# Optimization experiments

Measured on AMD Instinct MI355X. Metric: run time of the kernel, lower is better.

The kernel has to match this reference:

```python
import jax, jax.numpy as jnp
import numpy as np

TAU = 0.05


def _normalize(x):
    return x / jnp.linalg.norm(x, axis=-1, keepdims=True)


def setup_inputs() -> dict:
    key = jax.random.key(0)
    ks = jax.random.split(key, 7)
    D, S, Q, N, P = 256, 64, 4096, 16384, 1024
    return {
        "article_emb": jax.random.normal(ks[0], (D,), dtype=jnp.float32),
        "section_embs": jax.random.normal(ks[1], (S, D), dtype=jnp.float32),
        "question_embs": jax.random.normal(ks[2], (Q, D), dtype=jnp.float32),
        "sentence_embs": jax.random.normal(ks[3], (N, D), dtype=jnp.float32),
        "paragraph_idx_for_question": jax.random.randint(ks[4], (Q,), 0, P, dtype=jnp.int32),
        "section_idx_for_question": jax.random.randint(ks[5], (Q,), 0, S, dtype=jnp.int32),
        "sent_paragraph_idx": jax.random.randint(ks[6], (N,), 0, P, dtype=jnp.int32),
        "num_paragraphs": P,
    }


def reference(article_emb, section_embs, question_embs, sentence_embs,
              paragraph_idx_for_question, section_idx_for_question,
              sent_paragraph_idx, num_paragraphs):
    tau = TAU
    dt = question_embs.dtype
    # normalize (article is normalized in the original but unused in the loss; AT_loss == 0)
    _ = _normalize(article_emb)
    sec = _normalize(section_embs)   # [S, D]
    que = _normalize(question_embs)  # [Q, D]
    sen = _normalize(sentence_embs)  # [N, D]
    Q, N = que.shape[0], sen.shape[0]
    S = sec.shape[0]

    # ---------- QS debiased InfoNCE ----------
    sim_qs = jnp.matmul(que, sen.T) / tau              # [Q, N]
    exp_qs = jnp.exp(sim_qs)                           # [Q, N]
    pos = paragraph_idx_for_question[:, None] == sent_paragraph_idx[None, :]  # [Q, N]
    M = pos.sum(axis=1)                                # positives per question
    Nn = N - M                                         # negatives per question
    sum_pos = jnp.where(pos, exp_qs, 0.0).sum(axis=1)
    sum_neg = exp_qs.sum(axis=1) - sum_pos
    eta_plus = 1.0 / max(int(num_paragraphs), 1)
    eta_minus = 1.0 - eta_plus
    min_val = jnp.exp(jnp.asarray(-1.0 / tau, dtype=dt))
    M_f = jnp.maximum(M, 1).astype(dt)
    Nn_f = jnp.maximum(Nn, 1).astype(dt)
    g = jnp.maximum((sum_neg / Nn_f - eta_plus * sum_pos / M_f) / eta_minus, min_val)  # [Q]
    valid = (M > 0) & (Nn > 0)                         # [Q]
    # -log(numer / (numer + N_neg * g)) = -(sim - log(denom))
    denom_qs = exp_qs + (Nn.astype(dt) * g)[:, None]
    log_ratio_qs = sim_qs - jnp.log(denom_qs)
    mask_qs = pos & valid[:, None]
    total_qs = jnp.where(valid, M, 0).sum()
    qs_loss = -jnp.where(mask_qs, log_ratio_qs, 0.0).sum()
    qs_loss = jnp.where(total_qs > 0, qs_loss / total_qs.astype(dt), jnp.asarray(0.0, dt))

    # ---------- SQ InfoNCE ----------
    sim_sq = jnp.matmul(sec, que.T) / tau              # [S, Q]
    exp_sq = jnp.exp(sim_sq)
    posq = section_idx_for_question[None, :] == jnp.arange(S)[:, None]  # [S, Q]
    Mq = posq.sum(axis=1)
    Nnq = Q - Mq
    sum_neg_q = exp_sq.sum(axis=1) - jnp.where(posq, exp_sq, 0.0).sum(axis=1)  # [S]
    log_ratio_sq = sim_sq - jnp.log(exp_sq + sum_neg_q[:, None])
    validq = (Mq > 0) & (Nnq > 0)
    mask_sq = posq & validq[:, None]
    total_sq = jnp.where(validq, Mq, 0).sum()
    sq_loss = -jnp.where(mask_sq, log_ratio_sq, 0.0).sum()
    sq_loss = jnp.where(total_sq > 0, sq_loss / total_sq.astype(dt), jnp.asarray(0.0, dt))

    return qs_loss + sq_loss
```

## Files before the change

kernel.cpp:

```cpp
#include <hip/hip_runtime.h>
#include <hip/hip_bf16.h>
#include <math.h>

#define D 256
#define INV_TAU 20.0f
#define CAP 64
#define PBUF 128

typedef __attribute__((ext_vector_type(4))) float f32x4;
typedef __attribute__((ext_vector_type(8))) short bf16x8_t;

#define GLOAD16(gp, lp) \
    __builtin_amdgcn_global_load_lds((const __attribute__((address_space(1))) void*)(gp), \
                                     (__attribute__((address_space(3))) void*)(lp), 16, 0, 0)

__device__ __forceinline__ unsigned short f2bf(float f) {
    union { float f; unsigned u; } v; v.f = f;
    unsigned r = v.u + 0x7FFFu + ((v.u >> 16) & 1u);
    return (unsigned short)(r >> 16);
}

__global__ void norm_all(const float* __restrict__ que, const float* __restrict__ sen,
                         const float* __restrict__ sec,
                         unsigned short* __restrict__ queb, unsigned short* __restrict__ senb,
                         unsigned short* __restrict__ secb, int Q, int N, int S) {
    int r = blockIdx.x * 4 + (threadIdx.x >> 6);
    int lane = threadIdx.x & 63;
    if (r >= Q + N + S) return;
    const float* src; unsigned short* dst; int row;
    if (r < Q) { src = que; dst = queb; row = r; }
    else if (r < Q + N) { src = sen; dst = senb; row = r - Q; }
    else { src = sec; dst = secb; row = r - Q - N; }
    const float4* p = (const float4*)(src + (size_t)row * D);
    float4 v = p[lane];
    float ss = v.x * v.x + v.y * v.y + v.z * v.z + v.w * v.w;
    #pragma unroll
    for (int m = 1; m < 64; m <<= 1) ss += __shfl_xor(ss, m);
    float rn = rsqrtf(ss);
    ushort4 o;
    o.x = f2bf(v.x * rn); o.y = f2bf(v.y * rn); o.z = f2bf(v.z * rn); o.w = f2bf(v.w * rn);
    *(ushort4*)(dst + (size_t)row * D + lane * 4) = o;
}

__global__ __launch_bounds__(256, 4)
void qs_sq(const unsigned short* __restrict__ queb, const unsigned short* __restrict__ senb,
           const unsigned short* __restrict__ secb,
           const int* __restrict__ pidq, const int* __restrict__ pidn,
           const int* __restrict__ sidx, int Q,
           float* __restrict__ partial, int* __restrict__ cnt, float* __restrict__ pos_s,
           float* __restrict__ sq_all, float* __restrict__ sq_pos, int* __restrict__ sq_m,
           float* __restrict__ simq) {
    __shared__ unsigned short As[2][128 * 32];
    __shared__ unsigned short Bs[2][128 * 32];
    __shared__ int pqs[128];
    __shared__ int pns[128];
    __shared__ float sums[2][128];
    __shared__ int lcnt;
    __shared__ int lq[PBUF];
    __shared__ float lsv[PBUF];

    const int tid = threadIdx.x;
    const int lane = tid & 63;
    const int cl = lane & 15;
    const int g = lane >> 4;
    const int wid = tid >> 6;

    if (blockIdx.y == 0) {
        if ((int)blockIdx.x >= (Q >> 7)) return;
        const int q0 = blockIdx.x * 128;
        const int qw = q0 + wid * 32;
        f32x4 acc[4][2];
        #pragma unroll
        for (int si = 0; si < 4; ++si)
            #pragma unroll
            for (int qi = 0; qi < 2; ++qi)
                acc[si][qi] = (f32x4){0.f, 0.f, 0.f, 0.f};
        const unsigned short* abase = secb + (size_t)cl * D + g * 8;
        const unsigned short* bbase = queb + (size_t)(qw + cl) * D + g * 8;
        #pragma unroll
        for (int kk = 0; kk < 8; ++kk) {
            const int k0 = kk * 32;
            bf16x8_t af[4], bq[2];
            #pragma unroll
            for (int si = 0; si < 4; ++si)
                af[si] = *(const bf16x8_t*)(abase + si * 16 * D + k0);
            #pragma unroll
            for (int qi = 0; qi < 2; ++qi)
                bq[qi] = *(const bf16x8_t*)(bbase + qi * 16 * D + k0);
            #pragma unroll
            for (int si = 0; si < 4; ++si)
                #pragma unroll
                for (int qi = 0; qi < 2; ++qi)
                    acc[si][qi] = __builtin_amdgcn_mfma_f32_16x16x32_bf16(af[si], bq[qi], acc[si][qi], 0, 0, 0);
        }
        int sidxv[2];
        sidxv[0] = sidx[qw + cl];
        sidxv[1] = sidx[qw + 16 + cl];
        #pragma unroll
        for (int si = 0; si < 4; ++si) {
            float pa[4] = {0.f, 0.f, 0.f, 0.f};
            #pragma unroll
            for (int qi = 0; qi < 2; ++qi) {
                #pragma unroll
                for (int j = 0; j < 4; ++j) {
                    int srow = si * 16 + g * 4 + j;
                    float sv = acc[si][qi][j] * INV_TAU;
                    float e = __expf(sv);
                    pa[j] += e;
                    if (sidxv[qi] == srow) {
                        int q = qw + qi * 16 + cl;
                        simq[q] = sv;
                        atomicAdd(&sq_pos[srow], e);
                        atomicAdd(&sq_m[srow], 1);
                    }
                }
            }
            #pragma unroll
            for (int j = 0; j < 4; ++j) {
                float a = pa[j];
                #pragma unroll
                for (int msk = 1; msk < 16; msk <<= 1) a += __shfl_xor(a, msk);
                if (cl == 0) atomicAdd(&sq_all[si * 16 + g * 4 + j], a);
            }
        }
        return;
    }

    const int wr = wid >> 1, wc = wid & 1;
    const int n0 = blockIdx.x * 128;
    const int q0 = (blockIdx.y - 1) * 128;

    if (tid < 128) pqs[tid] = pidq[q0 + tid];
    else           pns[tid - 128] = pidn[n0 + tid - 128];
    if (tid == 0) lcnt = 0;
    __syncthreads();

    int cid0 = (2 * wid) * 64 + lane;
    int cid1 = (2 * wid + 1) * 64 + lane;
    const unsigned short* qa0 = queb + (size_t)(q0 + (cid0 >> 2)) * D + (cid0 & 3) * 8;
    const unsigned short* qa1 = queb + (size_t)(q0 + (cid1 >> 2)) * D + (cid1 & 3) * 8;
    const unsigned short* sb0 = senb + (size_t)(n0 + (cid0 >> 2)) * D + (cid0 & 3) * 8;
    const unsigned short* sb1 = senb + (size_t)(n0 + (cid1 >> 2)) * D + (cid1 & 3) * 8;
    const int ld0 = (2 * wid) * 512;
    const int ld1 = (2 * wid + 1) * 512;

#define STAGE(buf, k0) do { \
    GLOAD16(qa0 + (k0), &As[buf][ld0]); \
    GLOAD16(qa1 + (k0), &As[buf][ld1]); \
    GLOAD16(sb0 + (k0), &Bs[buf][ld0]); \
    GLOAD16(sb1 + (k0), &Bs[buf][ld1]); \
} while (0)

    f32x4 acc[4][4];
    #pragma unroll
    for (int m = 0; m < 4; ++m)
        #pragma unroll
        for (int n = 0; n < 4; ++n)
            acc[m][n] = (f32x4){0.f, 0.f, 0.f, 0.f};

    STAGE(0, 0);
    #pragma unroll
    for (int ks = 0; ks < 8; ++ks) {
        const int cur = ks & 1;
        if (ks < 7) {
            STAGE(cur ^ 1, (ks + 1) * 32);
            asm volatile("s_waitcnt vmcnt(4)" ::: "memory");
        } else {
            asm volatile("s_waitcnt vmcnt(0)" ::: "memory");
        }
        __builtin_amdgcn_s_barrier();
        bf16x8_t af[4], bg[4];
        #pragma unroll
        for (int m = 0; m < 4; ++m) {
            int r = wr * 64 + m * 16 + cl;
            af[m] = *(const bf16x8_t*)&As[cur][r * 32 + g * 8];
        }
        #pragma unroll
        for (int n = 0; n < 4; ++n) {
            int r = wc * 64 + n * 16 + cl;
            bg[n] = *(const bf16x8_t*)&Bs[cur][r * 32 + g * 8];
        }
        #pragma unroll
        for (int m = 0; m < 4; ++m)
            #pragma unroll
            for (int n = 0; n < 4; ++n)
                acc[m][n] = __builtin_amdgcn_mfma_f32_16x16x32_bf16(af[m], bg[n], acc[m][n], 0, 0, 0);
        if (ks < 7) __builtin_amdgcn_s_barrier();
    }
#undef STAGE

    #pragma unroll
    for (int m = 0; m < 4; ++m) {
        float se[4] = {0.f, 0.f, 0.f, 0.f};
        int pqr[4];
        #pragma unroll
        for (int j = 0; j < 4; ++j) pqr[j] = pqs[wr * 64 + m * 16 + g * 4 + j];
        #pragma unroll
        for (int n = 0; n < 4; ++n) {
            const int pcol = pns[wc * 64 + n * 16 + cl];
            #pragma unroll
            for (int j = 0; j < 4; ++j) {
                float s = acc[m][n][j] * INV_TAU;
                float e = __expf(s);
                se[j] += e;
                if (pqr[j] == pcol) {
                    int li = atomicAdd(&lcnt, 1);
                    if (li < PBUF) { lq[li] = q0 + wr * 64 + m * 16 + g * 4 + j; lsv[li] = s; }
                }
            }
        }
        #pragma unroll
        for (int j = 0; j < 4; ++j) {
            float a = se[j];
            #pragma unroll
            for (int msk = 1; msk < 16; msk <<= 1) a += __shfl_xor(a, msk);
            if (cl == 0) sums[wc][wr * 64 + m * 16 + g * 4 + j] = a;
        }
    }
    __syncthreads();
    if (tid < 128)
        partial[(size_t)blockIdx.x * Q + q0 + tid] = sums[0][tid] + sums[1][tid];
    int nc = lcnt < PBUF ? lcnt : PBUF;
    for (int i = tid; i < nc; i += 256) {
        int q = lq[i];
        int idx = atomicAdd(&cnt[q], 1);
        if (idx < CAP) pos_s[(size_t)q * CAP + idx] = lsv[i];
    }
}

__global__ __launch_bounds__(256)
void finish(const float* __restrict__ partial, int NB,
            const int* __restrict__ cnt, const float* __restrict__ pos_s,
            const int* __restrict__ sidx, const float* __restrict__ simq,
            const float* __restrict__ sq_all, const float* __restrict__ sq_pos,
            const int* __restrict__ sq_m,
            const int* __restrict__ npp, int Qn, int Ntot,
            float* __restrict__ bpart) {
    __shared__ float fred[4][4];
    const int tid = threadIdx.x, lane = tid & 63, wid = tid >> 6;
    const int q = blockIdx.x * 4 + wid;

    float Sa = 0.f;
    for (int nb = lane; nb < NB; nb += 64) Sa += partial[(size_t)nb * Qn + q];
    #pragma unroll
    for (int m = 1; m < 64; m <<= 1) Sa += __shfl_xor(Sa, m);

    int M = cnt[q];
    int mc = M < CAP ? M : CAP;
    float s = 0.f, e = 0.f;
    if (lane < mc) { s = pos_s[(size_t)q * CAP + lane]; e = __expf(s); }
    float Sp = e;
    #pragma unroll
    for (int m = 1; m < 64; m <<= 1) Sp += __shfl_xor(Sp, m);

    int Nn = Ntot - M;
    int P = npp[0];
    float eta_p = 1.0f / (float)(P > 1 ? P : 1);
    float eta_m = 1.0f - eta_p;
    float Mf = (float)(M > 1 ? M : 1);
    float Nnf = (float)(Nn > 1 ? Nn : 1);
    float gg = fmaxf(((Sa - Sp) / Nnf - eta_p * Sp / Mf) / eta_m, __expf(-INV_TAU));
    float c = (float)Nn * gg;

    float contrib = (lane < mc) ? (s - __logf(e + c)) : 0.f;
    #pragma unroll
    for (int m = 1; m < 64; m <<= 1) contrib += __shfl_xor(contrib, m);

    if (lane == 0) {
        float qs_num = 0.f, qs_cnt = 0.f, sq_num = 0.f, sq_cnt = 0.f;
        if (M > 0 && Nn > 0) { qs_num = contrib; qs_cnt = (float)M; }
        int sct = sidx[q];
        int Mq = sq_m[sct];
        if (Mq > 0 && (Qn - Mq) > 0) {
            float sv = simq[q];
            float sumneg = sq_all[sct] - sq_pos[sct];
            sq_num = sv - __logf(__expf(sv) + sumneg);
            sq_cnt = 1.f;
        }
        fred[wid][0] = qs_num; fred[wid][1] = qs_cnt;
        fred[wid][2] = sq_num; fred[wid][3] = sq_cnt;
    }
    __syncthreads();
    if (tid < 4) {
        float v = fred[0][tid] + fred[1][tid] + fred[2][tid] + fred[3][tid];
        bpart[(size_t)blockIdx.x * 4 + tid] = v;
    }
}

__global__ void combine2(const float* __restrict__ bpart, int nblk, float* __restrict__ out) {
    __shared__ float r2[4][4];
    const int tid = threadIdx.x, lane = tid & 63, wid = tid >> 6;
    float v[4] = {0.f, 0.f, 0.f, 0.f};
    for (int i = tid; i < nblk; i += 256) {
        #pragma unroll
        for (int c2 = 0; c2 < 4; ++c2) v[c2] += bpart[(size_t)i * 4 + c2];
    }
    #pragma unroll
    for (int m = 1; m < 64; m <<= 1)
        #pragma unroll
        for (int c2 = 0; c2 < 4; ++c2) v[c2] += __shfl_xor(v[c2], m);
    if (lane == 0) {
        #pragma unroll
        for (int c2 = 0; c2 < 4; ++c2) r2[wid][c2] = v[c2];
    }
    __syncthreads();
    if (tid == 0) {
        float qs_num = r2[0][0] + r2[1][0] + r2[2][0] + r2[3][0];
        float qs_cnt = r2[0][1] + r2[1][1] + r2[2][1] + r2[3][1];
        float sq_num = r2[0][2] + r2[1][2] + r2[2][2] + r2[3][2];
        float sq_cnt = r2[0][3] + r2[1][3] + r2[2][3] + r2[3][3];
        float qs = qs_cnt > 0.f ? -qs_num / qs_cnt : 0.f;
        float sq = sq_cnt > 0.f ? -sq_num / sq_cnt : 0.f;
        out[0] = qs + sq;
    }
}

extern "C" void kernel_launch(void* const* d_in, const int* in_sizes, int n_in,
                              void* d_out, int out_size, void* d_ws, size_t ws_size,
                              hipStream_t stream) {
    const float* sec = (const float*)d_in[1];
    const float* que = (const float*)d_in[2];
    const float* sen = (const float*)d_in[3];
    const int* pidq = (const int*)d_in[4];
    const int* sidx = (const int*)d_in[5];
    const int* pidn = (const int*)d_in[6];
    const int* npp = (const int*)d_in[7];
    const int S = in_sizes[1] / D;
    const int Q = in_sizes[2] / D;
    const int N = in_sizes[3] / D;
    const int NB = N / 128;
    const int FBLK = Q / 4;

    char* p = (char*)d_ws;
    unsigned short* queb = (unsigned short*)p; p += (size_t)Q * D * 2;
    unsigned short* senb = (unsigned short*)p; p += (size_t)N * D * 2;
    unsigned short* secb = (unsigned short*)p; p += (size_t)S * D * 2;
    float* simq = (float*)p; p += (size_t)Q * 4;
    float* pos_s = (float*)p; p += (size_t)Q * CAP * 4;
    float* partial = (float*)p; p += (size_t)NB * Q * 4;
    float* bpart = (float*)p; p += (size_t)FBLK * 4 * 4;
    char* z0 = p;
    int* cnt = (int*)p; p += (size_t)Q * 4;
    float* sq_all = (float*)p; p += (size_t)S * 4;
    float* sq_pos = (float*)p; p += (size_t)S * 4;
    int* sq_m = (int*)p; p += (size_t)S * 4;
    size_t zbytes = (size_t)(p - z0);

    hipMemsetAsync(z0, 0, zbytes, stream);
    norm_all<<<(Q + N + S + 3) / 4, 256, 0, stream>>>(que, sen, sec, queb, senb, secb, Q, N, S);
    qs_sq<<<dim3(NB, Q / 128 + 1), 256, 0, stream>>>(queb, senb, secb, pidq, pidn, sidx, Q,
                                                     partial, cnt, pos_s,
                                                     sq_all, sq_pos, sq_m, simq);
    finish<<<FBLK, 256, 0, stream>>>(partial, NB, cnt, pos_s, sidx, simq,
                                     sq_all, sq_pos, sq_m, npp, Q, N, bpart);
    combine2<<<1, 256, 0, stream>>>(bpart, FBLK, (float*)d_out);
}
```

Before: 100.6 us.

## Widen QS GEMM tile to 128x256 and XOR-swizzle LDS layout

Doubles the sentence dimension of each QS block tile from 128 to 256 columns, so every wave computes a 64x128 sub-tile with 32 MFMA accumulators and the question tile is reused across twice as many sentences. Global-to-LDS loads and LDS fragment reads now use an XOR swizzle on the 16-byte chunk index to cut LDS bank conflicts. Launch bounds drop to 2 waves per SIMD to fit the larger register footprint. The grid and per-block partial count halve, which reduces parallelism and occupancy in exchange for more reuse.

```diff
diff --git a/kernel.cpp b/kernel.cpp
--- a/kernel.cpp
+++ b/kernel.cpp
@@ -42,7 +42,7 @@
     *(ushort4*)(dst + (size_t)row * D + lane * 4) = o;
 }
 
-__global__ __launch_bounds__(256, 4)
+__global__ __launch_bounds__(256, 2)
 void qs_sq(const unsigned short* __restrict__ queb, const unsigned short* __restrict__ senb,
            const unsigned short* __restrict__ secb,
            const int* __restrict__ pidq, const int* __restrict__ pidn,
@@ -51,9 +51,9 @@
            float* __restrict__ sq_all, float* __restrict__ sq_pos, int* __restrict__ sq_m,
            float* __restrict__ simq) {
     __shared__ unsigned short As[2][128 * 32];
-    __shared__ unsigned short Bs[2][128 * 32];
+    __shared__ unsigned short Bs[2][256 * 32];
     __shared__ int pqs[128];
-    __shared__ int pns[128];
+    __shared__ int pns[256];
     __shared__ float sums[2][128];
     __shared__ int lcnt;
     __shared__ int lq[PBUF];
@@ -127,36 +127,59 @@
     }
 
     const int wr = wid >> 1, wc = wid & 1;
-    const int n0 = blockIdx.x * 128;
+    const int n0 = blockIdx.x * 256;
     const int q0 = (blockIdx.y - 1) * 128;
 
+    pns[tid] = pidn[n0 + tid];
     if (tid < 128) pqs[tid] = pidq[q0 + tid];
-    else           pns[tid - 128] = pidn[n0 + tid - 128];
     if (tid == 0) lcnt = 0;
     __syncthreads();
 
-    int cid0 = (2 * wid) * 64 + lane;
-    int cid1 = (2 * wid + 1) * 64 + lane;
-    const unsigned short* qa0 = queb + (size_t)(q0 + (cid0 >> 2)) * D + (cid0 & 3) * 8;
-    const unsigned short* qa1 = queb + (size_t)(q0 + (cid1 >> 2)) * D + (cid1 & 3) * 8;
-    const unsigned short* sb0 = senb + (size_t)(n0 + (cid0 >> 2)) * D + (cid0 & 3) * 8;
-    const unsigned short* sb1 = senb + (size_t)(n0 + (cid1 >> 2)) * D + (cid1 & 3) * 8;
-    const int ld0 = (2 * wid) * 512;
-    const int ld1 = (2 * wid + 1) * 512;
+    const unsigned short* qa[2];
+    const unsigned short* sb[4];
+    int ldA[2], ldB[4];
+    #pragma unroll
+    for (int j = 0; j < 2; ++j) {
+        int p = wid * 128 + j * 64 + lane;
+        int r = p >> 2, c = p & 3;
+        qa[j] = queb + (size_t)(q0 + r) * D + ((c ^ (r & 3)) << 3);
+        ldA[j] = (wid * 128 + j * 64) * 8;
+    }
+    #pragma unroll
+    for (int j = 0; j < 4; ++j) {
+        int p = wid * 256 + j * 64 + lane;
+        int r = p >> 2, c = p & 3;
+        sb[j] = senb + (size_t)(n0 + r) * D + ((c ^ (r & 3)) << 3);
+        ldB[j] = (wid * 256 + j * 64) * 8;
+    }
 
 #define STAGE(buf, k0) do { \
-    GLOAD16(qa0 + (k0), &As[buf][ld0]); \
-    GLOAD16(qa1 + (k0), &As[buf][ld1]); \
-    GLOAD16(sb0 + (k0), &Bs[buf][ld0]); \
-    GLOAD16(sb1 + (k0), &Bs[buf][ld1]); \
+    GLOAD16(qa[0] + (k0), &As[buf][ldA[0]]); \
+    GLOAD16(qa[1] + (k0), &As[buf][ldA[1]]); \
+    GLOAD16(sb[0] + (k0), &Bs[buf][ldB[0]]); \
+    GLOAD16(sb[1] + (k0), &Bs[buf][ldB[1]]); \
+    GLOAD16(sb[2] + (k0), &Bs[buf][ldB[2]]); \
+    GLOAD16(sb[3] + (k0), &Bs[buf][ldB[3]]); \
 } while (0)
 
-    f32x4 acc[4][4];
+    f32x4 acc[4][8];
     #pragma unroll
     for (int m = 0; m < 4; ++m)
         #pragma unroll
-        for (int n = 0; n < 4; ++n)
+        for (int n = 0; n < 8; ++n)
             acc[m][n] = (f32x4){0.f, 0.f, 0.f, 0.f};
+
+    int offA[4], offB[8];
+    #pragma unroll
+    for (int m = 0; m < 4; ++m) {
+        int r = wr * 64 + m * 16 + cl;
+        offA[m] = r * 32 + ((g ^ (r & 3)) << 3);
+    }
+    #pragma unroll
+    for (int n = 0; n < 8; ++n) {
+        int r = wc * 128 + n * 16 + cl;
+        offB[n] = r * 32 + ((g ^ (r & 3)) << 3);
+    }
 
     STAGE(0, 0);
     #pragma unroll
@@ -164,26 +187,20 @@
         const int cur = ks & 1;
         if (ks < 7) {
             STAGE(cur ^ 1, (ks + 1) * 32);
-            asm volatile("s_waitcnt vmcnt(4)" ::: "memory");
+            asm volatile("s_waitcnt vmcnt(6)" ::: "memory");
         } else {
             asm volatile("s_waitcnt vmcnt(0)" ::: "memory");
         }
         __builtin_amdgcn_s_barrier();
-        bf16x8_t af[4], bg[4];
-        #pragma unroll
-        for (int m = 0; m < 4; ++m) {
-            int r = wr * 64 + m * 16 + cl;
-            af[m] = *(const bf16x8_t*)&As[cur][r * 32 + g * 8];
-        }
-        #pragma unroll
-        for (int n = 0; n < 4; ++n) {
-            int r = wc * 64 + n * 16 + cl;
-            bg[n] = *(const bf16x8_t*)&Bs[cur][r * 32 + g * 8];
-        }
+        bf16x8_t af[4], bg[8];
+        #pragma unroll
+        for (int m = 0; m < 4; ++m) af[m] = *(const bf16x8_t*)&As[cur][offA[m]];
+        #pragma unroll
+        for (int n = 0; n < 8; ++n) bg[n] = *(const bf16x8_t*)&Bs[cur][offB[n]];
         #pragma unroll
         for (int m = 0; m < 4; ++m)
             #pragma unroll
-            for (int n = 0; n < 4; ++n)
+            for (int n = 0; n < 8; ++n)
                 acc[m][n] = __builtin_amdgcn_mfma_f32_16x16x32_bf16(af[m], bg[n], acc[m][n], 0, 0, 0);
         if (ks < 7) __builtin_amdgcn_s_barrier();
     }
@@ -196,8 +213,8 @@
         #pragma unroll
         for (int j = 0; j < 4; ++j) pqr[j] = pqs[wr * 64 + m * 16 + g * 4 + j];
         #pragma unroll
-        for (int n = 0; n < 4; ++n) {
-            const int pcol = pns[wc * 64 + n * 16 + cl];
+        for (int n = 0; n < 8; ++n) {
+            const int pcol = pns[wc * 128 + n * 16 + cl];
             #pragma unroll
             for (int j = 0; j < 4; ++j) {
                 float s = acc[m][n][j] * INV_TAU;
@@ -328,7 +345,7 @@
     const int S = in_sizes[1] / D;
     const int Q = in_sizes[2] / D;
     const int N = in_sizes[3] / D;
-    const int NB = N / 128;
+    const int NB = N / 256;
     const int FBLK = Q / 4;
 
     char* p = (char*)d_ws;
```

Result: slower. 112.3 us (+11.7%).

## Keep query tile resident in LDS and loop over sentence splits per block

Applied to the files above, without the earlier changes.

The QS kernel now loads a whole 128x256 query tile into swizzled LDS once and iterates over a 1/16 slice of the sentences. Sentence fragments are read straight from global memory into registers, and exp-sums accumulate across iterations. This replaces 128-row partial sums per sentence tile with 16 split partials, which shrinks the partial buffer and the finish-kernel reduction, and it reuses the query tile. In exchange the grid is much smaller (32x17 blocks), occupancy drops to two waves per SIMD, and B operands are uncached global loads with no prefetch pipelining.

```diff
diff --git a/kernel.cpp b/kernel.cpp
--- a/kernel.cpp
+++ b/kernel.cpp
@@ -5,7 +5,8 @@
 #define D 256
 #define INV_TAU 20.0f
 #define CAP 64
-#define PBUF 128
+#define PBUF 384
+#define NSPLIT 16
 
 typedef __attribute__((ext_vector_type(4))) float f32x4;
 typedef __attribute__((ext_vector_type(8))) short bf16x8_t;
@@ -42,18 +43,16 @@
     *(ushort4*)(dst + (size_t)row * D + lane * 4) = o;
 }
 
-__global__ __launch_bounds__(256, 4)
+__global__ __launch_bounds__(256, 2)
 void qs_sq(const unsigned short* __restrict__ queb, const unsigned short* __restrict__ senb,
            const unsigned short* __restrict__ secb,
            const int* __restrict__ pidq, const int* __restrict__ pidn,
-           const int* __restrict__ sidx, int Q,
+           const int* __restrict__ sidx, int Q, int N,
            float* __restrict__ partial, int* __restrict__ cnt, float* __restrict__ pos_s,
            float* __restrict__ sq_all, float* __restrict__ sq_pos, int* __restrict__ sq_m,
            float* __restrict__ simq) {
-    __shared__ unsigned short As[2][128 * 32];
-    __shared__ unsigned short Bs[2][128 * 32];
+    __shared__ unsigned short As[128 * 256];
     __shared__ int pqs[128];
-    __shared__ int pns[128];
     __shared__ float sums[2][128];
     __shared__ int lcnt;
     __shared__ int lq[PBUF];
@@ -66,7 +65,6 @@
     const int wid = tid >> 6;
 
     if (blockIdx.y == 0) {
-        if ((int)blockIdx.x >= (Q >> 7)) return;
         const int q0 = blockIdx.x * 128;
         const int qw = q0 + wid * 32;
         f32x4 acc[4][2];
@@ -127,99 +125,98 @@
     }
 
     const int wr = wid >> 1, wc = wid & 1;
-    const int n0 = blockIdx.x * 128;
-    const int q0 = (blockIdx.y - 1) * 128;
+    const int q0 = blockIdx.x * 128;
+    const int split = blockIdx.y - 1;
+    const int n0base = split * (N / NSPLIT);
+    const int niter = (N / NSPLIT) >> 7;
 
     if (tid < 128) pqs[tid] = pidq[q0 + tid];
-    else           pns[tid - 128] = pidn[n0 + tid - 128];
     if (tid == 0) lcnt = 0;
+
+    {
+        const unsigned short* asrc = queb + (size_t)(q0 + (tid >> 5)) * D
+                                   + (((tid & 31) ^ (tid >> 5)) << 3);
+        #pragma unroll
+        for (int j = 0; j < 16; ++j)
+            GLOAD16(asrc + j * 8 * D, &As[(j * 256 + wid * 64) * 8]);
+    }
     __syncthreads();
 
-    int cid0 = (2 * wid) * 64 + lane;
-    int cid1 = (2 * wid + 1) * 64 + lane;
-    const unsigned short* qa0 = queb + (size_t)(q0 + (cid0 >> 2)) * D + (cid0 & 3) * 8;
-    const unsigned short* qa1 = queb + (size_t)(q0 + (cid1 >> 2)) * D + (cid1 & 3) * 8;
-    const unsigned short* sb0 = senb + (size_t)(n0 + (cid0 >> 2)) * D + (cid0 & 3) * 8;
-    const unsigned short* sb1 = senb + (size_t)(n0 + (cid1 >> 2)) * D + (cid1 & 3) * 8;
-    const int ld0 = (2 * wid) * 512;
-    const int ld1 = (2 * wid + 1) * 512;
-
-#define STAGE(buf, k0) do { \
-    GLOAD16(qa0 + (k0), &As[buf][ld0]); \
-    GLOAD16(qa1 + (k0), &As[buf][ld1]); \
-    GLOAD16(sb0 + (k0), &Bs[buf][ld0]); \
-    GLOAD16(sb1 + (k0), &Bs[buf][ld1]); \
-} while (0)
-
-    f32x4 acc[4][4];
+    int pqr[16];
     #pragma unroll
     for (int m = 0; m < 4; ++m)
         #pragma unroll
+        for (int j = 0; j < 4; ++j)
+            pqr[m * 4 + j] = pqs[wr * 64 + m * 16 + g * 4 + j];
+
+    float se[16];
+    #pragma unroll
+    for (int i = 0; i < 16; ++i) se[i] = 0.f;
+
+    int abase0 = (wr * 64 + cl) * 256;
+
+    for (int ni = 0; ni < niter; ++ni) {
+        const int n0 = n0base + ni * 128;
+        const unsigned short* bp[4];
+        #pragma unroll
         for (int n = 0; n < 4; ++n)
-            acc[m][n] = (f32x4){0.f, 0.f, 0.f, 0.f};
-
-    STAGE(0, 0);
-    #pragma unroll
-    for (int ks = 0; ks < 8; ++ks) {
-        const int cur = ks & 1;
-        if (ks < 7) {
-            STAGE(cur ^ 1, (ks + 1) * 32);
-            asm volatile("s_waitcnt vmcnt(4)" ::: "memory");
-        } else {
-            asm volatile("s_waitcnt vmcnt(0)" ::: "memory");
-        }
-        __builtin_amdgcn_s_barrier();
-        bf16x8_t af[4], bg[4];
+            bp[n] = senb + (size_t)(n0 + wc * 64 + n * 16 + cl) * D + g * 8;
+
+        f32x4 acc[4][4];
+        #pragma unroll
+        for (int m = 0; m < 4; ++m)
+            #pragma unroll
+            for (int n = 0; n < 4; ++n)
+                acc[m][n] = (f32x4){0.f, 0.f, 0.f, 0.f};
+
+        #pragma unroll
+        for (int kk = 0; kk < 8; ++kk) {
+            const int ct = ((kk * 4 + g) ^ (cl & 7)) << 3;
+            bf16x8_t af[4], bg[4];
+            #pragma unroll
+            for (int n = 0; n < 4; ++n)
+                bg[n] = *(const bf16x8_t*)(bp[n] + kk * 32);
+            #pragma unroll
+            for (int m = 0; m < 4; ++m)
+                af[m] = *(const bf16x8_t*)&As[abase0 + m * 4096 + ct];
+            #pragma unroll
+            for (int m = 0; m < 4; ++m)
+                #pragma unroll
+                for (int n = 0; n < 4; ++n)
+                    acc[m][n] = __builtin_amdgcn_mfma_f32_16x16x32_bf16(af[m], bg[n], acc[m][n], 0, 0, 0);
+        }
+
+        int pcol[4];
+        #pragma unroll
+        for (int n = 0; n < 4; ++n) pcol[n] = pidn[n0 + wc * 64 + n * 16 + cl];
         #pragma unroll
         for (int m = 0; m < 4; ++m) {
-            int r = wr * 64 + m * 16 + cl;
-            af[m] = *(const bf16x8_t*)&As[cur][r * 32 + g * 8];
-        }
-        #pragma unroll
-        for (int n = 0; n < 4; ++n) {
-            int r = wc * 64 + n * 16 + cl;
-            bg[n] = *(const bf16x8_t*)&Bs[cur][r * 32 + g * 8];
-        }
-        #pragma unroll
-        for (int m = 0; m < 4; ++m)
-            #pragma unroll
-            for (int n = 0; n < 4; ++n)
-                acc[m][n] = __builtin_amdgcn_mfma_f32_16x16x32_bf16(af[m], bg[n], acc[m][n], 0, 0, 0);
-        if (ks < 7) __builtin_amdgcn_s_barrier();
-    }
-#undef STAGE
-
-    #pragma unroll
-    for (int m = 0; m < 4; ++m) {
-        float se[4] = {0.f, 0.f, 0.f, 0.f};
-        int pqr[4];
-        #pragma unroll
-        for (int j = 0; j < 4; ++j) pqr[j] = pqs[wr * 64 + m * 16 + g * 4 + j];
-        #pragma unroll
-        for (int n = 0; n < 4; ++n) {
-            const int pcol = pns[wc * 64 + n * 16 + cl];
-            #pragma unroll
-            for (int j = 0; j < 4; ++j) {
-                float s = acc[m][n][j] * INV_TAU;
-                float e = __expf(s);
-                se[j] += e;
-                if (pqr[j] == pcol) {
-                    int li = atomicAdd(&lcnt, 1);
-                    if (li < PBUF) { lq[li] = q0 + wr * 64 + m * 16 + g * 4 + j; lsv[li] = s; }
+            #pragma unroll
+            for (int n = 0; n < 4; ++n) {
+                #pragma unroll
+                for (int j = 0; j < 4; ++j) {
+                    float s = acc[m][n][j] * INV_TAU;
+                    float e = __expf(s);
+                    se[m * 4 + j] += e;
+                    if (pqr[m * 4 + j] == pcol[n]) {
+                        int li = atomicAdd(&lcnt, 1);
+                        if (li < PBUF) { lq[li] = q0 + wr * 64 + m * 16 + g * 4 + j; lsv[li] = s; }
+                    }
                 }
             }
         }
-        #pragma unroll
-        for (int j = 0; j < 4; ++j) {
-            float a = se[j];
-            #pragma unroll
-            for (int msk = 1; msk < 16; msk <<= 1) a += __shfl_xor(a, msk);
-            if (cl == 0) sums[wc][wr * 64 + m * 16 + g * 4 + j] = a;
-        }
+    }
+
+    #pragma unroll
+    for (int i = 0; i < 16; ++i) {
+        float a = se[i];
+        #pragma unroll
+        for (int msk = 1; msk < 16; msk <<= 1) a += __shfl_xor(a, msk);
+        if (cl == 0) sums[wc][wr * 64 + (i >> 2) * 16 + g * 4 + (i & 3)] = a;
     }
     __syncthreads();
     if (tid < 128)
-        partial[(size_t)blockIdx.x * Q + q0 + tid] = sums[0][tid] + sums[1][tid];
+        partial[(size_t)split * Q + q0 + tid] = sums[0][tid] + sums[1][tid];
     int nc = lcnt < PBUF ? lcnt : PBUF;
     for (int i = tid; i < nc; i += 256) {
         int q = lq[i];
@@ -328,7 +325,6 @@
     const int S = in_sizes[1] / D;
     const int Q = in_sizes[2] / D;
     const int N = in_sizes[3] / D;
-    const int NB = N / 128;
     const int FBLK = Q / 4;
 
     char* p = (char*)d_ws;
@@ -337,7 +333,7 @@
     unsigned short* secb = (unsigned short*)p; p += (size_t)S * D * 2;
     float* simq = (float*)p; p += (size_t)Q * 4;
     float* pos_s = (float*)p; p += (size_t)Q * CAP * 4;
-    float* partial = (float*)p; p += (size_t)NB * Q * 4;
+    float* partial = (float*)p; p += (size_t)NSPLIT * Q * 4;
     float* bpart = (float*)p; p += (size_t)FBLK * 4 * 4;
     char* z0 = p;
     int* cnt = (int*)p; p += (size_t)Q * 4;
@@ -348,10 +344,10 @@
 
     hipMemsetAsync(z0, 0, zbytes, stream);
     norm_all<<<(Q + N + S + 3) / 4, 256, 0, stream>>>(que, sen, sec, queb, senb, secb, Q, N, S);
-    qs_sq<<<dim3(NB, Q / 128 + 1), 256, 0, stream>>>(queb, senb, secb, pidq, pidn, sidx, Q,
-                                                     partial, cnt, pos_s,
-                                                     sq_all, sq_pos, sq_m, simq);
-    finish<<<FBLK, 256, 0, stream>>>(partial, NB, cnt, pos_s, sidx, simq,
+    qs_sq<<<dim3(Q / 128, NSPLIT + 1), 256, 0, stream>>>(queb, senb, secb, pidq, pidn, sidx,
+                                                         Q, N, partial, cnt, pos_s,
+                                                         sq_all, sq_pos, sq_m, simq);
+    finish<<<FBLK, 256, 0, stream>>>(partial, NSPLIT, cnt, pos_s, sidx, simq,
                                      sq_all, sq_pos, sq_m, npp, Q, N, bpart);
     combine2<<<1, 256, 0, stream>>>(bpart, FBLK, (float*)d_out);
 }
```

Measured after the change: 123.5 us. +22.8%, slower.

## Enlarge QS tiles to 256x256 with 512 threads, swizzled LDS and exp2

Applied to the files above, without the earlier changes.

The QS similarity kernel moves from 128x128 tiles with 4 waves to 256x256 tiles with 8 waves, each wave computing 128x64. The goal is to raise operand reuse and cut the number of blocks and partial-sum slices. Global-to-LDS loads and fragment reads now use a matching XOR swizzle to reduce LDS bank conflicts. The exponential uses exp2 with 1/tau and log2(e) folded into one constant. The larger register footprint (32 accumulators plus 32 row sums) may lower occupancy, and the block decode hardcodes 64 N-tiles, which only matches N=16384.

```diff
diff --git a/kernel.cpp b/kernel.cpp
--- a/kernel.cpp
+++ b/kernel.cpp
@@ -5,7 +5,8 @@
 #define D 256
 #define INV_TAU 20.0f
 #define CAP 64
-#define PBUF 128
+#define PBUF 256
+#define K2 (20.0f * 1.442695040888963f)
 
 typedef __attribute__((ext_vector_type(4))) float f32x4;
 typedef __attribute__((ext_vector_type(8))) short bf16x8_t;
@@ -42,7 +43,7 @@
     *(ushort4*)(dst + (size_t)row * D + lane * 4) = o;
 }
 
-__global__ __launch_bounds__(256, 4)
+__global__ __launch_bounds__(512, 2)
 void qs_sq(const unsigned short* __restrict__ queb, const unsigned short* __restrict__ senb,
            const unsigned short* __restrict__ secb,
            const int* __restrict__ pidq, const int* __restrict__ pidn,
@@ -50,11 +51,11 @@
            float* __restrict__ partial, int* __restrict__ cnt, float* __restrict__ pos_s,
            float* __restrict__ sq_all, float* __restrict__ sq_pos, int* __restrict__ sq_m,
            float* __restrict__ simq) {
-    __shared__ unsigned short As[2][128 * 32];
-    __shared__ unsigned short Bs[2][128 * 32];
-    __shared__ int pqs[128];
-    __shared__ int pns[128];
-    __shared__ float sums[2][128];
+    __shared__ unsigned short As[2][256 * 32];
+    __shared__ unsigned short Bs[2][256 * 32];
+    __shared__ int pqs[256];
+    __shared__ int pns[256];
+    __shared__ float sums[4][256];
     __shared__ int lcnt;
     __shared__ int lq[PBUF];
     __shared__ float lsv[PBUF];
@@ -64,10 +65,11 @@
     const int cl = lane & 15;
     const int g = lane >> 4;
     const int wid = tid >> 6;
-
-    if (blockIdx.y == 0) {
-        if ((int)blockIdx.x >= (Q >> 7)) return;
-        const int q0 = blockIdx.x * 128;
+    const int bid = blockIdx.x;
+    const int nsq = Q >> 8;
+
+    if (bid < nsq) {
+        const int q0 = bid * 256;
         const int qw = q0 + wid * 32;
         f32x4 acc[4][2];
         #pragma unroll
@@ -126,37 +128,47 @@
         return;
     }
 
-    const int wr = wid >> 1, wc = wid & 1;
-    const int n0 = blockIdx.x * 128;
-    const int q0 = (blockIdx.y - 1) * 128;
-
-    if (tid < 128) pqs[tid] = pidq[q0 + tid];
-    else           pns[tid - 128] = pidn[n0 + tid - 128];
+    const int qbid = bid - nsq;
+    const int qt = qbid >> 6;
+    const int nt = qbid & 63;
+    const int wrow = wid >> 2;
+    const int wcol = wid & 3;
+    const int q0 = qt * 256;
+    const int n0 = nt * 256;
+
+    if (tid < 256) pqs[tid] = pidq[q0 + tid];
+    else           pns[tid - 256] = pidn[n0 + tid - 256];
     if (tid == 0) lcnt = 0;
     __syncthreads();
 
-    int cid0 = (2 * wid) * 64 + lane;
-    int cid1 = (2 * wid + 1) * 64 + lane;
-    const unsigned short* qa0 = queb + (size_t)(q0 + (cid0 >> 2)) * D + (cid0 & 3) * 8;
-    const unsigned short* qa1 = queb + (size_t)(q0 + (cid1 >> 2)) * D + (cid1 & 3) * 8;
-    const unsigned short* sb0 = senb + (size_t)(n0 + (cid0 >> 2)) * D + (cid0 & 3) * 8;
-    const unsigned short* sb1 = senb + (size_t)(n0 + (cid1 >> 2)) * D + (cid1 & 3) * 8;
-    const int ld0 = (2 * wid) * 512;
-    const int ld1 = (2 * wid + 1) * 512;
+    const int swz = (((tid & 3) ^ ((tid >> 3) & 3)) << 3);
+    const unsigned short* qa0 = queb + (size_t)(q0 + (tid >> 2)) * D + swz;
+    const unsigned short* sb0 = senb + (size_t)(n0 + (tid >> 2)) * D + swz;
+    const int ld0 = wid * 512;
+    const int ld1 = 4096 + wid * 512;
 
 #define STAGE(buf, k0) do { \
     GLOAD16(qa0 + (k0), &As[buf][ld0]); \
-    GLOAD16(qa1 + (k0), &As[buf][ld1]); \
+    GLOAD16(qa0 + 128 * D + (k0), &As[buf][ld1]); \
     GLOAD16(sb0 + (k0), &Bs[buf][ld0]); \
-    GLOAD16(sb1 + (k0), &Bs[buf][ld1]); \
+    GLOAD16(sb0 + 128 * D + (k0), &Bs[buf][ld1]); \
 } while (0)
 
-    f32x4 acc[4][4];
-    #pragma unroll
-    for (int m = 0; m < 4; ++m)
+    f32x4 acc[8][4];
+    #pragma unroll
+    for (int m = 0; m < 8; ++m)
         #pragma unroll
         for (int n = 0; n < 4; ++n)
             acc[m][n] = (f32x4){0.f, 0.f, 0.f, 0.f};
+
+    const int xorv = (g ^ ((cl >> 1) & 3)) << 3;
+    int offA[8], offB[4];
+    #pragma unroll
+    for (int m = 0; m < 8; ++m)
+        offA[m] = (wrow * 128 + m * 16 + cl) * 32 + xorv;
+    #pragma unroll
+    for (int n = 0; n < 4; ++n)
+        offB[n] = (wcol * 64 + n * 16 + cl) * 32 + xorv;
 
     STAGE(0, 0);
     #pragma unroll
@@ -169,19 +181,13 @@
             asm volatile("s_waitcnt vmcnt(0)" ::: "memory");
         }
         __builtin_amdgcn_s_barrier();
-        bf16x8_t af[4], bg[4];
-        #pragma unroll
-        for (int m = 0; m < 4; ++m) {
-            int r = wr * 64 + m * 16 + cl;
-            af[m] = *(const bf16x8_t*)&As[cur][r * 32 + g * 8];
-        }
-        #pragma unroll
-        for (int n = 0; n < 4; ++n) {
-            int r = wc * 64 + n * 16 + cl;
-            bg[n] = *(const bf16x8_t*)&Bs[cur][r * 32 + g * 8];
-        }
-        #pragma unroll
-        for (int m = 0; m < 4; ++m)
+        bf16x8_t af[8], bg[4];
+        #pragma unroll
+        for (int m = 0; m < 8; ++m) af[m] = *(const bf16x8_t*)&As[cur][offA[m]];
+        #pragma unroll
+        for (int n = 0; n < 4; ++n) bg[n] = *(const bf16x8_t*)&Bs[cur][offB[n]];
+        #pragma unroll
+        for (int m = 0; m < 8; ++m)
             #pragma unroll
             for (int n = 0; n < 4; ++n)
                 acc[m][n] = __builtin_amdgcn_mfma_f32_16x16x32_bf16(af[m], bg[n], acc[m][n], 0, 0, 0);
@@ -189,39 +195,45 @@
     }
 #undef STAGE
 
-    #pragma unroll
-    for (int m = 0; m < 4; ++m) {
-        float se[4] = {0.f, 0.f, 0.f, 0.f};
+    float se[32];
+    #pragma unroll
+    for (int i = 0; i < 32; ++i) se[i] = 0.f;
+    #pragma unroll
+    for (int m = 0; m < 8; ++m) {
         int pqr[4];
         #pragma unroll
-        for (int j = 0; j < 4; ++j) pqr[j] = pqs[wr * 64 + m * 16 + g * 4 + j];
+        for (int j = 0; j < 4; ++j) pqr[j] = pqs[wrow * 128 + m * 16 + g * 4 + j];
         #pragma unroll
         for (int n = 0; n < 4; ++n) {
-            const int pcol = pns[wc * 64 + n * 16 + cl];
+            const int pcol = pns[wcol * 64 + n * 16 + cl];
             #pragma unroll
             for (int j = 0; j < 4; ++j) {
-                float s = acc[m][n][j] * INV_TAU;
-                float e = __expf(s);
-                se[j] += e;
+                float e = __builtin_amdgcn_exp2f(acc[m][n][j] * K2);
+                se[m * 4 + j] += e;
                 if (pqr[j] == pcol) {
                     int li = atomicAdd(&lcnt, 1);
-                    if (li < PBUF) { lq[li] = q0 + wr * 64 + m * 16 + g * 4 + j; lsv[li] = s; }
+                    if (li < PBUF) {
+                        lq[li] = q0 + wrow * 128 + m * 16 + g * 4 + j;
+                        lsv[li] = acc[m][n][j] * INV_TAU;
+                    }
                 }
             }
         }
-        #pragma unroll
-        for (int j = 0; j < 4; ++j) {
-            float a = se[j];
-            #pragma unroll
-            for (int msk = 1; msk < 16; msk <<= 1) a += __shfl_xor(a, msk);
-            if (cl == 0) sums[wc][wr * 64 + m * 16 + g * 4 + j] = a;
-        }
+    }
+    #pragma unroll
+    for (int i = 0; i < 32; ++i) {
+        float a = se[i];
+        #pragma unroll
+        for (int msk = 1; msk < 16; msk <<= 1) a += __shfl_xor(a, msk);
+        if (cl == 0)
+            sums[wcol][wrow * 128 + (i >> 2) * 16 + g * 4 + (i & 3)] = a;
     }
     __syncthreads();
-    if (tid < 128)
-        partial[(size_t)blockIdx.x * Q + q0 + tid] = sums[0][tid] + sums[1][tid];
+    if (tid < 256)
+        partial[(size_t)nt * Q + q0 + tid] =
+            sums[0][tid] + sums[1][tid] + sums[2][tid] + sums[3][tid];
     int nc = lcnt < PBUF ? lcnt : PBUF;
-    for (int i = tid; i < nc; i += 256) {
+    for (int i = tid; i < nc; i += 512) {
         int q = lq[i];
         int idx = atomicAdd(&cnt[q], 1);
         if (idx < CAP) pos_s[(size_t)q * CAP + idx] = lsv[i];
@@ -229,7 +241,7 @@
 }
 
 __global__ __launch_bounds__(256)
-void finish(const float* __restrict__ partial, int NB,
+void finish(const float* __restrict__ partial, int NSLICE,
             const int* __restrict__ cnt, const float* __restrict__ pos_s,
             const int* __restrict__ sidx, const float* __restrict__ simq,
             const float* __restrict__ sq_all, const float* __restrict__ sq_pos,
@@ -241,7 +253,7 @@
     const int q = blockIdx.x * 4 + wid;
 
     float Sa = 0.f;
-    for (int nb = lane; nb < NB; nb += 64) Sa += partial[(size_t)nb * Qn + q];
+    for (int nb = lane; nb < NSLICE; nb += 64) Sa += partial[(size_t)nb * Qn + q];
     #pragma unroll
     for (int m = 1; m < 64; m <<= 1) Sa += __shfl_xor(Sa, m);
 
@@ -328,7 +340,7 @@
     const int S = in_sizes[1] / D;
     const int Q = in_sizes[2] / D;
     const int N = in_sizes[3] / D;
-    const int NB = N / 128;
+    const int NSLICE = N / 256;
     const int FBLK = Q / 4;
 
     char* p = (char*)d_ws;
@@ -337,7 +349,7 @@
     unsigned short* secb = (unsigned short*)p; p += (size_t)S * D * 2;
     float* simq = (float*)p; p += (size_t)Q * 4;
     float* pos_s = (float*)p; p += (size_t)Q * CAP * 4;
-    float* partial = (float*)p; p += (size_t)NB * Q * 4;
+    float* partial = (float*)p; p += (size_t)NSLICE * Q * 4;
     float* bpart = (float*)p; p += (size_t)FBLK * 4 * 4;
     char* z0 = p;
     int* cnt = (int*)p; p += (size_t)Q * 4;
@@ -348,10 +360,10 @@
 
     hipMemsetAsync(z0, 0, zbytes, stream);
     norm_all<<<(Q + N + S + 3) / 4, 256, 0, stream>>>(que, sen, sec, queb, senb, secb, Q, N, S);
-    qs_sq<<<dim3(NB, Q / 128 + 1), 256, 0, stream>>>(queb, senb, secb, pidq, pidn, sidx, Q,
-                                                     partial, cnt, pos_s,
-                                                     sq_all, sq_pos, sq_m, simq);
-    finish<<<FBLK, 256, 0, stream>>>(partial, NB, cnt, pos_s, sidx, simq,
+    qs_sq<<<Q / 256 + (Q / 256) * (N / 256), 512, 0, stream>>>(queb, senb, secb, pidq, pidn,
+                                                               sidx, Q, partial, cnt, pos_s,
+                                                               sq_all, sq_pos, sq_m, simq);
+    finish<<<FBLK, 256, 0, stream>>>(partial, NSLICE, cnt, pos_s, sidx, simq,
                                      sq_all, sq_pos, sq_m, npp, Q, N, bpart);
     combine2<<<1, 256, 0, stream>>>(bpart, FBLK, (float*)d_out);
 }
```

Result: slower. 120.8 us (+20.1%).
